# Optimization experiments

Hardware: AMD Instinct MI355X
Metric: run time of the kernel (lower is better)

The kernel has to match this reference:

```python
import jax, jax.numpy as jnp
import numpy as np

N_STUDENT = 100000
N_COURSE = 20000
N_EDGES = 1000000
HIDDEN = 128


def setup_inputs() -> dict:
    key = jax.random.key(0)
    ks = jax.random.split(key, 8)
    scale = 1.0 / np.sqrt(2 * HIDDEN)
    return {
        "z_student": jax.random.normal(ks[0], (N_STUDENT, HIDDEN), dtype=jnp.float32),
        "z_course": jax.random.normal(ks[1], (N_COURSE, HIDDEN), dtype=jnp.float32),
        "row": jax.random.randint(ks[2], (N_EDGES,), 0, N_STUDENT, dtype=jnp.int64),
        "col": jax.random.randint(ks[3], (N_EDGES,), 0, N_COURSE, dtype=jnp.int64),
        "W1": jax.random.normal(ks[4], (2 * HIDDEN, HIDDEN), dtype=jnp.float32) * scale,
        "b1": jnp.zeros((HIDDEN,), dtype=jnp.float32),
        "W2": jax.random.normal(ks[5], (HIDDEN, 1), dtype=jnp.float32) * (1.0 / np.sqrt(HIDDEN)),
        "b2": jnp.zeros((1,), dtype=jnp.float32),
    }


def reference(z_student, z_course, row, col, W1, b1, W2, b2):
    # gather endpoint embeddings and concat along feature dim: [E, 2H]
    z = jnp.concatenate([z_student[row], z_course[col]], axis=-1)
    h = jax.nn.relu(z @ W1 + b1)   # [E, H]
    out = h @ W2 + b2              # [E, 1]
    return out.reshape(-1)
```

## Files before the change

kernel.cpp:

```cpp
#include <hip/hip_runtime.h>
#include <hip/hip_bf16.h>
#include <hip/hip_fp16.h>


typedef _Float16 half2v __attribute__((ext_vector_type(2)));
typedef _Float16 half8v __attribute__((ext_vector_type(8)));
typedef __fp16   fp16x2 __attribute__((ext_vector_type(2)));
typedef float    float4v __attribute__((ext_vector_type(4)));

#define NB 1024
#define EH 8448
#define EBLK_S 2048

__global__ __launch_bounds__(256) void k1_conv_hist(
    const float* __restrict__ W1, const float* __restrict__ W2,
    const int* __restrict__ row,
    _Float16* __restrict__ Wt, _Float16* __restrict__ w2h,
    unsigned* __restrict__ hist, int E)
{
    int b = blockIdx.x, t = threadIdx.x;
    if (b >= 9) {
        __shared__ unsigned h[NB];
        #pragma unroll
        for (int i = 0; i < 4; ++i) h[t + i * 256] = 0;
        __syncthreads();
        long b0 = (long)(b - 9) * EH;
        for (int i = 0; i < 33; ++i) {
            long e = b0 + i * 256 + t;
            if (e < E) atomicAdd(&h[row[e] >> 7], 1u);
        }
        __syncthreads();
        #pragma unroll
        for (int i = 0; i < 4; ++i) {
            unsigned v = h[t + i * 256];
            if (v) atomicAdd(&hist[t + i * 256], v);
        }
        return;
    }
    if (b == 8) { if (t < 128) w2h[t] = (_Float16)W2[t]; return; }
    __shared__ _Float16 lds[32][136];
    int h2 = b >> 2, n0 = (b & 3) * 32;
    for (int i = 0; i < 16; ++i) {
        int idx = i * 256 + t;
        int k = idx >> 5, nn = idx & 31;
        lds[nn][k] = (_Float16)W1[(h2 * 128 + k) * 128 + n0 + nn];
    }
    __syncthreads();
    for (int j = 0; j < 2; ++j) {
        int idx = j * 256 + t;
        int nn = idx >> 4, kc = idx & 15;
        half8v v;
        #pragma unroll
        for (int q = 0; q < 8; ++q) v[q] = lds[nn][kc * 8 + q];
        *(half8v*)&Wt[((h2 * 128 + n0 + nn) * 128) + kc * 8] = v;
    }
}

__global__ __launch_bounds__(1024) void k2_scan(const unsigned* __restrict__ hist,
                                                unsigned* __restrict__ bucketStart,
                                                unsigned* __restrict__ cursor, int E)
{
    __shared__ unsigned s[NB];
    int t = threadIdx.x;
    unsigned v = hist[t];
    s[t] = v;
    __syncthreads();
    for (int d = 1; d < NB; d <<= 1) {
        unsigned x = (t >= d) ? s[t - d] : 0u;
        __syncthreads();
        s[t] += x;
        __syncthreads();
    }
    unsigned excl = s[t] - v;
    bucketStart[t] = excl;
    cursor[t] = excl;
    if (t == 0) bucketStart[NB] = (unsigned)E;
}

__global__ __launch_bounds__(256) void k3_scatter_gemm(
    const int* __restrict__ row, const int* __restrict__ col,
    unsigned* __restrict__ cursor, uint2* __restrict__ perm, int E, int nbs_s,
    const float* __restrict__ Zs, const float* __restrict__ Zc,
    const _Float16* __restrict__ Wt, const float* __restrict__ b1,
    _Float16* __restrict__ Us, _Float16* __restrict__ Uc,
    int Ms, int Mc, int nbs)
{
    const int t = threadIdx.x;
    if (blockIdx.x < (unsigned)nbs_s) {
        __shared__ unsigned h[NB];
        __shared__ unsigned base[NB];
        #pragma unroll
        for (int i = 0; i < 4; ++i) h[t + i * 256] = 0;
        __syncthreads();
        long b0 = (long)blockIdx.x * EBLK_S;
        int sk[8], rr[8], cc[8];
        #pragma unroll
        for (int i = 0; i < 8; ++i) {
            long e = b0 + i * 256 + t;
            if (e < E) {
                rr[i] = row[e]; cc[i] = col[e];
                sk[i] = rr[i] >> 7;
                atomicAdd(&h[sk[i]], 1u);
            } else sk[i] = -1;
        }
        __syncthreads();
        #pragma unroll
        for (int i = 0; i < 4; ++i) {
            unsigned hv = h[t + i * 256];
            if (hv) base[t + i * 256] = atomicAdd(&cursor[t + i * 256], hv);
        }
        __syncthreads();
        #pragma unroll
        for (int i = 0; i < 4; ++i) h[t + i * 256] = 0;
        __syncthreads();
        #pragma unroll
        for (int i = 0; i < 8; ++i) {
            if (sk[i] >= 0) {
                unsigned off = atomicAdd(&h[sk[i]], 1u);
                unsigned pos = base[sk[i]] + off;
                long e = b0 + i * 256 + t;
                perm[pos] = make_uint2(((unsigned)(rr[i] & 127) << 15) | (unsigned)cc[i],
                                       (unsigned)e);
            }
        }
        return;
    }
    __shared__ uint4 ldsW[2048];
    const int bid = blockIdx.x - nbs_s;

    const float* Z; _Float16* U; const _Float16* W; int M, m0, addB;
    if (bid < nbs) { Z = Zs; U = Us; M = Ms; m0 = bid * 64;         W = Wt;         addB = 1; }
    else           { Z = Zc; U = Uc; M = Mc; m0 = (bid - nbs) * 64; W = Wt + 16384; addB = 0; }

    const uint4* Wv = (const uint4*)W;
    #pragma unroll
    for (int i = 0; i < 8; ++i) {
        int j = i * 256 + t;
        int n = j >> 4, ch = j & 15;
        ldsW[n * 16 + (ch ^ ((n >> 3) & 7))] = Wv[j];
    }
    __syncthreads();

    const int wave = t >> 6, lane = t & 63, quad = lane >> 4, l16 = lane & 15;
    int mrow = m0 + wave * 16 + l16;
    int mload = mrow < M ? mrow : M - 1;
    const float* zrow = Z + (long)mload * 128;

    float4v acc[8];
    #pragma unroll
    for (int nt = 0; nt < 8; ++nt) acc[nt] = (float4v)(0.0f);

    #pragma unroll
    for (int c = 0; c < 4; ++c) {
        const float4v* pa = (const float4v*)(zrow + c * 32 + quad * 8);
        float4v a0 = pa[0], a1 = pa[1];
        fp16x2 p[4];
        p[0] = __builtin_amdgcn_cvt_pkrtz(a0[0], a0[1]);
        p[1] = __builtin_amdgcn_cvt_pkrtz(a0[2], a0[3]);
        p[2] = __builtin_amdgcn_cvt_pkrtz(a1[0], a1[1]);
        p[3] = __builtin_amdgcn_cvt_pkrtz(a1[2], a1[3]);
        half8v af;
        __builtin_memcpy(&af, &p[0], 16);
        const int ch = c * 4 + quad;
        #pragma unroll
        for (int nt = 0; nt < 8; ++nt) {
            const int n = l16 * 8 + nt;
            const half8v* pb = (const half8v*)&ldsW[n * 16 + (ch ^ (l16 & 7))];
            acc[nt] = __builtin_amdgcn_mfma_f32_16x16x32_f16(af, *pb, acc[nt], 0, 0, 0);
        }
    }

    float bv[8];
    if (addB) {
        const float4v* pb1 = (const float4v*)(b1 + l16 * 8);
        float4v x0 = pb1[0], x1 = pb1[1];
        bv[0]=x0[0]; bv[1]=x0[1]; bv[2]=x0[2]; bv[3]=x0[3];
        bv[4]=x1[0]; bv[5]=x1[1]; bv[6]=x1[2]; bv[7]=x1[3];
    } else {
        #pragma unroll
        for (int i = 0; i < 8; ++i) bv[i] = 0.0f;
    }

    const int rbase = m0 + wave * 16 + quad * 4;
    #pragma unroll
    for (int r = 0; r < 4; ++r) {
        int rr2 = rbase + r;
        if (rr2 < M) {
            half8v o;
            #pragma unroll
            for (int nt = 0; nt < 8; ++nt) o[nt] = (_Float16)(acc[nt][r] + bv[nt]);
            *(half8v*)&U[(long)rr2 * 128 + l16 * 8] = o;
        }
    }
}

__global__ __launch_bounds__(256) void k4_edge(
    const uint2* __restrict__ perm, const unsigned* __restrict__ bucketStart,
    const _Float16* __restrict__ us, const _Float16* __restrict__ uc,
    const _Float16* __restrict__ w2h, const float* __restrict__ b2,
    float* __restrict__ out, int Ms)
{
    __shared__ uint4 lu[2048];
    const int t = threadIdx.x, b = blockIdx.x;
    const int r0 = b << 7;
    const uint4* usv = (const uint4*)us;
    #pragma unroll
    for (int i = 0; i < 8; ++i) {
        int j = t + i * 256;
        int rl = j >> 4, ch = j & 15;
        int r = r0 + rl; if (r >= Ms) r = Ms - 1;
        lu[rl * 16 + (ch ^ (rl & 15))] = usv[(long)r * 16 + ch];
    }
    const int sub = t & 7;
    const uint4* pw = ((const uint4*)w2h) + sub * 2;
    uint4 w0 = pw[0], w1 = pw[1];
    half2v W[8];
    *(uint4*)&W[0] = w0; *(uint4*)&W[4] = w1;
    const float b2v = b2[0];
    const half2v zero = {(_Float16)0, (_Float16)0};
    unsigned s0 = bucketStart[b], s1 = bucketStart[b + 1];
    __syncthreads();

    if (s0 >= s1) return;
    const unsigned cnt = s1 - s0;
    const uint4* ucv = (const uint4*)uc;

    unsigned k = t >> 3;
    uint2 pcA = perm[s0 + (k       < cnt ? k       : 0u)];
    uint2 pcB = perm[s0 + (k + 32u < cnt ? k + 32u : 0u)];
    uint4 U0, U1;
    {
        const uint4* pb = ucv + (long)(pcA.x & 32767u) * 16 + sub * 2;
        U0 = pb[0]; U1 = pb[1];
    }
    for (; k < cnt; k += 32u) {
        uint2 pcC = perm[s0 + (k + 64u < cnt ? k + 64u : 0u)];
        uint4 V0, V1;
        {
            const uint4* pb = ucv + (long)(pcB.x & 32767u) * 16 + sub * 2;
            V0 = pb[0]; V1 = pb[1];
        }
        unsigned rloc = pcA.x >> 15;
        int m = rloc & 15;
        uint4 a0 = lu[rloc * 16 + ((sub * 2) ^ m)];
        uint4 a1 = lu[rloc * 16 + ((sub * 2 + 1) ^ m)];

        half2v A[8], B[8];
        *(uint4*)&A[0] = a0; *(uint4*)&A[4] = a1;
        *(uint4*)&B[0] = U0; *(uint4*)&B[4] = U1;

        float s = 0.0f;
        #pragma unroll
        for (int i = 0; i < 8; ++i) {
            half2v h = A[i] + B[i];
            h = __builtin_elementwise_max(h, zero);
            s += (float)h[0] * (float)W[i][0];
            s += (float)h[1] * (float)W[i][1];
        }
        s += __shfl_xor(s, 1);
        s += __shfl_xor(s, 2);
        s += __shfl_xor(s, 4);
        if (sub == 0) out[pcA.y] = s + b2v;

        pcA = pcB; pcB = pcC; U0 = V0; U1 = V1;
    }
}

extern "C" void kernel_launch(void* const* d_in, const int* in_sizes, int n_in,
                              void* d_out, int out_size, void* d_ws, size_t ws_size,
                              hipStream_t stream) {
    const float* zs  = (const float*)d_in[0];
    const float* zc  = (const float*)d_in[1];
    const int*   row = (const int*)d_in[2];
    const int*   col = (const int*)d_in[3];
    const float* W1  = (const float*)d_in[4];
    const float* b1  = (const float*)d_in[5];
    const float* W2  = (const float*)d_in[6];
    const float* b2  = (const float*)d_in[7];
    float* out = (float*)d_out;

    const int Ms = in_sizes[0] / 128;
    const int Mc = in_sizes[1] / 128;
    const int E  = in_sizes[2];

    char* w = (char*)d_ws;
    _Float16* Wt     = (_Float16*)(w);
    _Float16* w2h    = (_Float16*)(w + 65536);
    unsigned* hist   = (unsigned*)(w + 66560);
    unsigned* bstart = (unsigned*)(w + 70656);
    unsigned* cursor = (unsigned*)(w + 75776);
    _Float16* us     = (_Float16*)(w + 81920);
    _Float16* uc     = (_Float16*)(w + 81920 + (size_t)Ms * 256);
    uint2*    perm   = (uint2*)(w + 81920 + (size_t)(Ms + Mc) * 256);

    const int nbs = (Ms + 63) / 64, nbc = (Mc + 63) / 64;
    const int nbh = (E + EH - 1) / EH;
    const int nbss = (E + EBLK_S - 1) / EBLK_S;
    const int nbuckets = (Ms + 127) >> 7;

    hipMemsetAsync(hist, 0, NB * 4, stream);
    k1_conv_hist<<<9 + nbh, 256, 0, stream>>>(W1, W2, row, Wt, w2h, hist, E);
    k2_scan<<<1, 1024, 0, stream>>>(hist, bstart, cursor, E);
    k3_scatter_gemm<<<nbss + nbs + nbc, 256, 0, stream>>>(row, col, cursor, perm, E, nbss,
                                                          zs, zc, Wt, b1, us, uc, Ms, Mc, nbs);
    k4_edge<<<nbuckets, 256, 0, stream>>>(perm, bstart, us, uc, w2h, b2, out, Ms);
}
```

Baseline: 191.9 us.

## Process multiple GEMM tiles per block with prefetch, split edge buckets across two blocks

The GEMM part of k3 now has each block handle four 64-row tiles, loading the weight matrix into LDS once and double-buffering the next tile's Z rows in registers while MFMA runs on the current one. The scatter blocks process 4096 edges each instead of 2048. LDS is unified into one shared array, and launch bounds request three blocks per CU. k4 launches two blocks per bucket, each handling half the bucket's edges; this doubles parallelism but also doubles the LDS staging of student rows per bucket.

```diff
diff --git a/kernel.cpp b/kernel.cpp
--- a/kernel.cpp
+++ b/kernel.cpp
@@ -10,7 +10,8 @@
 
 #define NB 1024
 #define EH 8448
-#define EBLK_S 2048
+#define EBLK_S 4096
+#define TPB 4
 
 __global__ __launch_bounds__(256) void k1_conv_hist(
     const float* __restrict__ W1, const float* __restrict__ W2,
@@ -77,25 +78,26 @@
     if (t == 0) bucketStart[NB] = (unsigned)E;
 }
 
-__global__ __launch_bounds__(256) void k3_scatter_gemm(
+__global__ __launch_bounds__(256, 3) void k3_scatter_gemm(
     const int* __restrict__ row, const int* __restrict__ col,
     unsigned* __restrict__ cursor, uint2* __restrict__ perm, int E, int nbs_s,
     const float* __restrict__ Zs, const float* __restrict__ Zc,
     const _Float16* __restrict__ Wt, const float* __restrict__ b1,
     _Float16* __restrict__ Us, _Float16* __restrict__ Uc,
-    int Ms, int Mc, int nbs)
+    int Ms, int Mc, int nbsg)
 {
+    __shared__ __align__(16) unsigned smem[8192];
     const int t = threadIdx.x;
     if (blockIdx.x < (unsigned)nbs_s) {
-        __shared__ unsigned h[NB];
-        __shared__ unsigned base[NB];
+        unsigned* h    = smem;
+        unsigned* base = smem + NB;
         #pragma unroll
         for (int i = 0; i < 4; ++i) h[t + i * 256] = 0;
         __syncthreads();
         long b0 = (long)blockIdx.x * EBLK_S;
-        int sk[8], rr[8], cc[8];
-        #pragma unroll
-        for (int i = 0; i < 8; ++i) {
+        int sk[16], rr[16], cc[16];
+        #pragma unroll
+        for (int i = 0; i < 16; ++i) {
             long e = b0 + i * 256 + t;
             if (e < E) {
                 rr[i] = row[e]; cc[i] = col[e];
@@ -114,7 +116,7 @@
         for (int i = 0; i < 4; ++i) h[t + i * 256] = 0;
         __syncthreads();
         #pragma unroll
-        for (int i = 0; i < 8; ++i) {
+        for (int i = 0; i < 16; ++i) {
             if (sk[i] >= 0) {
                 unsigned off = atomicAdd(&h[sk[i]], 1u);
                 unsigned pos = base[sk[i]] + off;
@@ -125,12 +127,12 @@
         }
         return;
     }
-    __shared__ uint4 ldsW[2048];
-    const int bid = blockIdx.x - nbs_s;
-
-    const float* Z; _Float16* U; const _Float16* W; int M, m0, addB;
-    if (bid < nbs) { Z = Zs; U = Us; M = Ms; m0 = bid * 64;         W = Wt;         addB = 1; }
-    else           { Z = Zc; U = Uc; M = Mc; m0 = (bid - nbs) * 64; W = Wt + 16384; addB = 0; }
+    uint4* ldsW = (uint4*)smem;
+    int gid = blockIdx.x - nbs_s;
+
+    const float* Z; _Float16* U; const _Float16* W; int M, tbase, addB;
+    if (gid < nbsg) { Z = Zs; U = Us; M = Ms; W = Wt;         addB = 1; tbase = gid * TPB; }
+    else { gid -= nbsg; Z = Zc; U = Uc; M = Mc; W = Wt + 16384; addB = 0; tbase = gid * TPB; }
 
     const uint4* Wv = (const uint4*)W;
     #pragma unroll
@@ -142,33 +144,6 @@
     __syncthreads();
 
     const int wave = t >> 6, lane = t & 63, quad = lane >> 4, l16 = lane & 15;
-    int mrow = m0 + wave * 16 + l16;
-    int mload = mrow < M ? mrow : M - 1;
-    const float* zrow = Z + (long)mload * 128;
-
-    float4v acc[8];
-    #pragma unroll
-    for (int nt = 0; nt < 8; ++nt) acc[nt] = (float4v)(0.0f);
-
-    #pragma unroll
-    for (int c = 0; c < 4; ++c) {
-        const float4v* pa = (const float4v*)(zrow + c * 32 + quad * 8);
-        float4v a0 = pa[0], a1 = pa[1];
-        fp16x2 p[4];
-        p[0] = __builtin_amdgcn_cvt_pkrtz(a0[0], a0[1]);
-        p[1] = __builtin_amdgcn_cvt_pkrtz(a0[2], a0[3]);
-        p[2] = __builtin_amdgcn_cvt_pkrtz(a1[0], a1[1]);
-        p[3] = __builtin_amdgcn_cvt_pkrtz(a1[2], a1[3]);
-        half8v af;
-        __builtin_memcpy(&af, &p[0], 16);
-        const int ch = c * 4 + quad;
-        #pragma unroll
-        for (int nt = 0; nt < 8; ++nt) {
-            const int n = l16 * 8 + nt;
-            const half8v* pb = (const half8v*)&ldsW[n * 16 + (ch ^ (l16 & 7))];
-            acc[nt] = __builtin_amdgcn_mfma_f32_16x16x32_f16(af, *pb, acc[nt], 0, 0, 0);
-        }
-    }
 
     float bv[8];
     if (addB) {
@@ -181,17 +156,60 @@
         for (int i = 0; i < 8; ++i) bv[i] = 0.0f;
     }
 
-    const int rbase = m0 + wave * 16 + quad * 4;
+    float4v buf[2][8];
+    #define LOADZ(dst, tile) do {                                              \
+        int mrow_ = (tile) * 64 + wave * 16 + l16;                             \
+        int mload_ = mrow_ < M ? mrow_ : M - 1;                                \
+        const float4v* p_ = (const float4v*)(Z + (long)mload_ * 128);          \
+        _Pragma("unroll")                                                      \
+        for (int c_ = 0; c_ < 4; ++c_) {                                       \
+            (dst)[2*c_]   = p_[c_*8 + quad*2];                                 \
+            (dst)[2*c_+1] = p_[c_*8 + quad*2 + 1];                             \
+        }                                                                      \
+    } while (0)
+
+    LOADZ(buf[0], tbase);
     #pragma unroll
-    for (int r = 0; r < 4; ++r) {
-        int rr2 = rbase + r;
-        if (rr2 < M) {
-            half8v o;
+    for (int tt = 0; tt < TPB; ++tt) {
+        const float4v* cur = buf[tt & 1];
+        if (tt + 1 < TPB) LOADZ(buf[(tt + 1) & 1], tbase + tt + 1);
+
+        float4v acc[8];
+        #pragma unroll
+        for (int nt = 0; nt < 8; ++nt) acc[nt] = (float4v)(0.0f);
+
+        #pragma unroll
+        for (int c = 0; c < 4; ++c) {
+            float4v a0 = cur[2*c], a1 = cur[2*c+1];
+            fp16x2 p[4];
+            p[0] = __builtin_amdgcn_cvt_pkrtz(a0[0], a0[1]);
+            p[1] = __builtin_amdgcn_cvt_pkrtz(a0[2], a0[3]);
+            p[2] = __builtin_amdgcn_cvt_pkrtz(a1[0], a1[1]);
+            p[3] = __builtin_amdgcn_cvt_pkrtz(a1[2], a1[3]);
+            half8v af;
+            __builtin_memcpy(&af, &p[0], 16);
+            const int ch = c * 4 + quad;
             #pragma unroll
-            for (int nt = 0; nt < 8; ++nt) o[nt] = (_Float16)(acc[nt][r] + bv[nt]);
-            *(half8v*)&U[(long)rr2 * 128 + l16 * 8] = o;
-        }
-    }
+            for (int nt = 0; nt < 8; ++nt) {
+                const int n = l16 * 8 + nt;
+                const half8v* pb = (const half8v*)&ldsW[n * 16 + (ch ^ (l16 & 7))];
+                acc[nt] = __builtin_amdgcn_mfma_f32_16x16x32_f16(af, *pb, acc[nt], 0, 0, 0);
+            }
+        }
+
+        const int rbase = (tbase + tt) * 64 + wave * 16 + quad * 4;
+        #pragma unroll
+        for (int r = 0; r < 4; ++r) {
+            int rr2 = rbase + r;
+            if (rr2 < M) {
+                half8v o;
+                #pragma unroll
+                for (int nt = 0; nt < 8; ++nt) o[nt] = (_Float16)(acc[nt][r] + bv[nt]);
+                *(half8v*)&U[(long)rr2 * 128 + l16 * 8] = o;
+            }
+        }
+    }
+    #undef LOADZ
 }
 
 __global__ __launch_bounds__(256) void k4_edge(
@@ -201,7 +219,8 @@
     float* __restrict__ out, int Ms)
 {
     __shared__ uint4 lu[2048];
-    const int t = threadIdx.x, b = blockIdx.x;
+    const int t = threadIdx.x;
+    const int b = blockIdx.x >> 1, half = blockIdx.x & 1;
     const int r0 = b << 7;
     const uint4* usv = (const uint4*)us;
     #pragma unroll
@@ -218,9 +237,14 @@
     *(uint4*)&W[0] = w0; *(uint4*)&W[4] = w1;
     const float b2v = b2[0];
     const half2v zero = {(_Float16)0, (_Float16)0};
-    unsigned s0 = bucketStart[b], s1 = bucketStart[b + 1];
+    unsigned s0b = bucketStart[b], s1b = bucketStart[b + 1];
     __syncthreads();
 
+    unsigned cntAll = s1b - s0b;
+    if (cntAll == 0) return;
+    unsigned hc = (cntAll + 1) >> 1;
+    unsigned s0 = s0b + half * hc;
+    unsigned s1 = s0 + hc; if (s1 > s1b) s1 = s1b;
     if (s0 >= s1) return;
     const unsigned cnt = s1 - s0;
     const uint4* ucv = (const uint4*)uc;
@@ -294,6 +318,8 @@
     uint2*    perm   = (uint2*)(w + 81920 + (size_t)(Ms + Mc) * 256);
 
     const int nbs = (Ms + 63) / 64, nbc = (Mc + 63) / 64;
+    const int nbsg = (nbs + TPB - 1) / TPB;
+    const int nbcg = (nbc + TPB - 1) / TPB;
     const int nbh = (E + EH - 1) / EH;
     const int nbss = (E + EBLK_S - 1) / EBLK_S;
     const int nbuckets = (Ms + 127) >> 7;
@@ -301,7 +327,7 @@
     hipMemsetAsync(hist, 0, NB * 4, stream);
     k1_conv_hist<<<9 + nbh, 256, 0, stream>>>(W1, W2, row, Wt, w2h, hist, E);
     k2_scan<<<1, 1024, 0, stream>>>(hist, bstart, cursor, E);
-    k3_scatter_gemm<<<nbss + nbs + nbc, 256, 0, stream>>>(row, col, cursor, perm, E, nbss,
-                                                          zs, zc, Wt, b1, us, uc, Ms, Mc, nbs);
-    k4_edge<<<nbuckets, 256, 0, stream>>>(perm, bstart, us, uc, w2h, b2, out, Ms);
-}
+    k3_scatter_gemm<<<nbss + nbsg + nbcg, 256, 0, stream>>>(row, col, cursor, perm, E, nbss,
+                                                            zs, zc, Wt, b1, us, uc, Ms, Mc, nbsg);
+    k4_edge<<<2 * nbuckets, 256, 0, stream>>>(perm, bstart, us, uc, w2h, b2, out, Ms);
+}
```

Result: faster. 178.3 us (-7.1%).
